# Kernel optimization log

Measured on AMD Instinct MI355X. Metric: run time of the kernel, lower is better.

The kernel has to match this reference:

```python
import jax, jax.numpy as jnp
import numpy as np

N_PARENTS = 4096   # parent clusters
K = 32             # points decoded per cluster
NEIGH = 128        # neigh_dec_size
FEAT = 256         # input_size (per-parent feature dim passed through)


def setup_inputs() -> dict:
    key = jax.random.key(0)
    ks = jax.random.split(key, 6)
    def lin(k, fan_in, fan_out):
        return jax.random.normal(k, (fan_in, fan_out), jnp.float32) / np.sqrt(fan_in).astype(np.float32)
    return {
        "input_features": jax.random.normal(ks[0], (N_PARENTS, NEIGH + FEAT), jnp.float32),
        # neighborhood decoder: Linear NEIGH -> K*3 (relative points)
        "W_dec": lin(ks[1], NEIGH, K * 3), "b_dec": jnp.zeros((K * 3,), jnp.float32),
        # fc chain: (FEAT+3) -> 512 -> 512 -> 256
        "W1": lin(ks[2], FEAT + 3, 512), "b1": jnp.zeros((512,), jnp.float32),
        "W2": lin(ks[3], 512, 512),      "b2": jnp.zeros((512,), jnp.float32),
        "W3": lin(ks[4], 512, 256),      "b3": jnp.zeros((256,), jnp.float32),
    }


def reference(input_features, W_dec, b_dec, W1, b1, W2, b2, W3, b3):
    # split: first NEIGH dims go to the neighborhood decoder, rest are parent features
    neigh_feats = input_features[:, :NEIGH]            # [N, NEIGH]
    features = input_features[:, NEIGH:]               # [N, FEAT]

    # neighborhood_dec: decode K relative 3D points per parent + cluster assignment
    relative_points = (neigh_feats @ W_dec + b_dec).reshape(-1, 3)   # [N*K, 3]
    cluster = jnp.repeat(jnp.arange(N_PARENTS, dtype=jnp.int32), K)  # [N*K]

    # gather parent features per point, concat with relative points
    features_dup = features[cluster]                                  # [N*K, FEAT]
    h = jnp.concatenate([features_dup, relative_points], axis=1)      # [N*K, FEAT+3]

    # chained Linear + ReLU (leaky=False)
    h = jax.nn.relu(h @ W1 + b1)
    h = jax.nn.relu(h @ W2 + b2)
    h = jax.nn.relu(h @ W3 + b3)
    return relative_points, h, cluster
```

## Files before the change

kernel.cpp:

```cpp
#include <hip/hip_runtime.h>
#include <hip/hip_bf16.h>

typedef unsigned short u16;
typedef unsigned int   u32;

#define NP     4096
#define NCH    131072
#define HBASE  393216
#define CLBASE 33947648

#define WS_W2F   0
#define WS_W3F   524288
#define WS_F1    1048576

using bf16x8 = __attribute__((ext_vector_type(8))) short;
using f32x4  = __attribute__((ext_vector_type(4))) float;

__device__ inline u32 pk2(float a, float b) {
  __hip_bfloat162 h = __float22bfloat162_rn(make_float2(a, b));
  return *reinterpret_cast<u32*>(&h);
}

__device__ inline int swz(int r, int cg) {
  return cg ^ (r & 7) ^ ((r >> 3) & 3);
}

__global__ __launch_bounds__(512, 2) void k_pre(const float* __restrict__ in_feats,
                                                const float* __restrict__ Wd,
                                                const float* __restrict__ bd,
                                                const float* __restrict__ W1,
                                                const float* __restrict__ b1,
                                                const float* __restrict__ W2,
                                                const float* __restrict__ W3,
                                                u16* __restrict__ w2f,
                                                u16* __restrict__ w3f,
                                                float* __restrict__ F1,
                                                float* __restrict__ out) {
  __shared__ __align__(16) char smem[69504];
  int b = blockIdx.x, tid = threadIdx.x;

  if (b < 256) {
    u16*   sh_a = (u16*)smem;
    float* b1s  = (float*)(smem + 8192);
    float* wdT  = (float*)(smem + 10240);
    float* ne   = (float*)(smem + 60928);
    float* bds  = (float*)(smem + 69120);
    int p0 = b * 16, lane = tid & 63, w = tid >> 6;
    b1s[tid] = b1[tid];
    if (tid < 96) bds[tid] = bd[tid];
    {
      int r = tid >> 5, k4 = (tid & 31) * 4;
      *(float4*)(ne + r * 128 + k4) = *(const float4*)(in_feats + (p0 + r) * 384 + k4);
    }
    {
      int r = tid >> 5, k0 = (tid & 31) * 8;
      const float4 v0 = *(const float4*)(in_feats + (p0 + r) * 384 + 128 + k0);
      const float4 v1 = *(const float4*)(in_feats + (p0 + r) * 384 + 128 + k0 + 4);
      uint4 o;
      o.x = pk2(v0.x, v0.y); o.y = pk2(v0.z, v0.w);
      o.z = pk2(v1.x, v1.y); o.w = pk2(v1.z, v1.w);
      int slot = (k0 >> 3) ^ (r & 7);
      *(uint4*)(sh_a + r * 256 + slot * 8) = o;
    }
    {
#pragma unroll
      for (int i = 0; i < 6; ++i) {
        int idx = i * 512 + tid;
        int k = idx / 24, c4 = (idx % 24) * 4;
        const float4 v = *(const float4*)(Wd + k * 96 + c4);
        wdT[(c4 + 0) * 132 + k] = v.x;
        wdT[(c4 + 1) * 132 + k] = v.y;
        wdT[(c4 + 2) * 132 + k] = v.z;
        wdT[(c4 + 3) * 132 + k] = v.w;
      }
    }
    __syncthreads();
#pragma unroll
    for (int j = 0; j < 3; ++j) {
      int u = j * 512 + tid;
      int p = u / 96, c = u - p * 96;
      const float4* nep = (const float4*)(ne + p * 128);
      const float4* wp  = (const float4*)(wdT + c * 132);
      float4 a4 = {0.f, 0.f, 0.f, 0.f};
#pragma unroll 8
      for (int kq = 0; kq < 32; ++kq) {
        const float4 av = nep[kq], bv = wp[kq];
        a4.x += av.x * bv.x; a4.y += av.y * bv.y;
        a4.z += av.z * bv.z; a4.w += av.w * bv.w;
      }
      out[(p0 + p) * 96 + c] = bds[c] + ((a4.x + a4.y) + (a4.z + a4.w));
    }
    f32x4 acc[4];
#pragma unroll
    for (int i = 0; i < 4; ++i) acc[i] = f32x4{0.f, 0.f, 0.f, 0.f};
    int col = lane & 15, q8 = (lane >> 4) * 8;
#pragma unroll
    for (int kc = 0; kc < 8; ++kc) {
      int slot = ((kc * 32 + q8) >> 3) ^ (col & 7);
      bf16x8 a = *(const bf16x8*)(sh_a + col * 256 + slot * 8);
#pragma unroll
      for (int nf = 0; nf < 4; ++nf) {
        const float* wp = W1 + (kc * 32 + q8) * 512 + (w * 4 + nf) * 16 + col;
        float v0 = wp[0],      v1 = wp[512],  v2 = wp[1024], v3 = wp[1536];
        float v4 = wp[2048],   v5 = wp[2560], v6 = wp[3072], v7 = wp[3584];
        union { bf16x8 v; u32 u[4]; } uu;
        uu.u[0] = pk2(v0, v1); uu.u[1] = pk2(v2, v3);
        uu.u[2] = pk2(v4, v5); uu.u[3] = pk2(v6, v7);
        acc[nf] = __builtin_amdgcn_mfma_f32_16x16x32_bf16(a, uu.v, acc[nf], 0, 0, 0);
      }
    }
    int rb = (lane >> 4) * 4;
#pragma unroll
    for (int nf = 0; nf < 4; ++nf) {
      int n = w * 64 + nf * 16 + col;
#pragma unroll
      for (int i = 0; i < 4; ++i)
        F1[(p0 + rb + i) * 512 + n] = acc[nf][i] + b1s[n];
    }
  } else if (b < 448) {
    float (*tile)[32][33] = (float (*)[32][33])smem;
    int h = tid >> 8, t = tid & 255;
    const float* src; u16* dst; int pitchN, g;
    if (b < 384) { g = (b - 256) * 2 + h; src = W2; dst = w2f; pitchN = 512; }
    else         { g = (b - 384) * 2 + h; src = W3; dst = w3f; pitchN = 256; }
    int kt = g & 15, nt = g >> 4;
    {
      int kk = t >> 3, n4 = (t & 7) * 4;
      const float4 v = *(const float4*)(src + (kt * 32 + kk) * pitchN + nt * 32 + n4);
      tile[h][kk][n4 + 0] = v.x; tile[h][kk][n4 + 1] = v.y;
      tile[h][kk][n4 + 2] = v.z; tile[h][kk][n4 + 3] = v.w;
    }
    __syncthreads();
    {
      int s = t >> 1, half = t & 1, fr = s >> 6, l = s & 63;
      int n_l = fr * 16 + (l & 15);
      int k_l = (l >> 4) * 8 + half * 4;
      uint2 o;
      o.x = pk2(tile[h][k_l + 0][n_l], tile[h][k_l + 1][n_l]);
      o.y = pk2(tile[h][k_l + 2][n_l], tile[h][k_l + 3][n_l]);
      int frag_id = (nt * 2 + fr) * 16 + kt;
      *(uint2*)(dst + frag_id * 512 + l * 8 + half * 4) = o;
    }
  } else {
    int idx = ((b - 448) * 512 + tid) * 4;
    float c = (float)(idx >> 5);
    float* p = out + CLBASE + idx;
    __builtin_nontemporal_store(c, p + 0);
    __builtin_nontemporal_store(c, p + 1);
    __builtin_nontemporal_store(c, p + 2);
    __builtin_nontemporal_store(c, p + 3);
  }
}

__global__ __launch_bounds__(512, 4) void k_main(const float* __restrict__ W1,
                                                 const float* __restrict__ b2,
                                                 const float* __restrict__ b3,
                                                 const u16* __restrict__ w2f,
                                                 const u16* __restrict__ w3f,
                                                 const float* __restrict__ F1,
                                                 float* __restrict__ out) {
  int blk = blockIdx.x;
  int tid = threadIdx.x, lane = tid & 63, w = tid >> 6;
  __shared__ u16 sh_h[64 * 512];
  __shared__ float f1s[1024], w1bs[1536], b2s[512], b3s[256], rels[192];

  f1s[tid]       = F1[blk * 1024 + tid];
  f1s[tid + 512] = F1[blk * 1024 + 512 + tid];
  w1bs[tid]        = W1[131072 + tid];
  w1bs[tid + 512]  = W1[131072 + 512 + tid];
  w1bs[tid + 1024] = W1[131072 + 1024 + tid];
  b2s[tid] = b2[tid];
  if (tid < 256) b3s[tid] = b3[tid];
  if (tid < 192) rels[tid] = out[blk * 192 + tid];
  __syncthreads();

  {
    int r = tid & 31, g = tid >> 5;
#pragma unroll
    for (int rr = 0; rr < 64; rr += 32) {
      int row = rr + r, pp = rr >> 5;
      float r0 = rels[row * 3 + 0], r1 = rels[row * 3 + 1], r2 = rels[row * 3 + 2];
#pragma unroll
      for (int gg = 0; gg < 4; ++gg) {
        int c8 = g * 8 + gg * 128;
        const float4 fa = *(const float4*)(f1s + pp * 512 + c8);
        const float4 fb = *(const float4*)(f1s + pp * 512 + c8 + 4);
        const float4 wa0 = *(const float4*)(w1bs + c8);
        const float4 wb0 = *(const float4*)(w1bs + c8 + 4);
        const float4 wa1 = *(const float4*)(w1bs + 512 + c8);
        const float4 wb1 = *(const float4*)(w1bs + 512 + c8 + 4);
        const float4 wa2 = *(const float4*)(w1bs + 1024 + c8);
        const float4 wb2 = *(const float4*)(w1bs + 1024 + c8 + 4);
        float v0 = fmaxf(fa.x + r0 * wa0.x + r1 * wa1.x + r2 * wa2.x, 0.f);
        float v1 = fmaxf(fa.y + r0 * wa0.y + r1 * wa1.y + r2 * wa2.y, 0.f);
        float v2 = fmaxf(fa.z + r0 * wa0.z + r1 * wa1.z + r2 * wa2.z, 0.f);
        float v3 = fmaxf(fa.w + r0 * wa0.w + r1 * wa1.w + r2 * wa2.w, 0.f);
        float v4 = fmaxf(fb.x + r0 * wb0.x + r1 * wb1.x + r2 * wb2.x, 0.f);
        float v5 = fmaxf(fb.y + r0 * wb0.y + r1 * wb1.y + r2 * wb2.y, 0.f);
        float v6 = fmaxf(fb.z + r0 * wb0.z + r1 * wb1.z + r2 * wb2.z, 0.f);
        float v7 = fmaxf(fb.w + r0 * wb0.w + r1 * wb1.w + r2 * wb2.w, 0.f);
        uint4 o;
        o.x = pk2(v0, v1); o.y = pk2(v2, v3);
        o.z = pk2(v4, v5); o.w = pk2(v6, v7);
        *(uint4*)(sh_h + row * 512 + swz(row, c8 >> 3) * 8) = o;
      }
    }
  }
  __syncthreads();

  int col = lane & 15, q8 = (lane >> 4) * 8;

  f32x4 acc2[4][4];
#pragma unroll
  for (int mf = 0; mf < 4; ++mf)
#pragma unroll
    for (int nf = 0; nf < 4; ++nf) acc2[mf][nf] = f32x4{0.f, 0.f, 0.f, 0.f};
  {
    const u16* w2p = w2f + (size_t)(w * 4 * 16) * 512 + lane * 8;
    bf16x8 bufA[4], bufB[4];
#pragma unroll
    for (int nf = 0; nf < 4; ++nf) bufA[nf] = *(const bf16x8*)(w2p + nf * 16 * 512);
#pragma unroll 2
    for (int kc = 0; kc < 16; ++kc) {
      const bf16x8* cur = (kc & 1) ? bufB : bufA;
      bf16x8* nxt = (kc & 1) ? bufA : bufB;
      if (kc < 15) {
#pragma unroll
        for (int nf = 0; nf < 4; ++nf)
          nxt[nf] = *(const bf16x8*)(w2p + (nf * 16 + kc + 1) * 512);
      }
      int cb = (kc * 32 + q8) >> 3;
#pragma unroll
      for (int mf = 0; mf < 4; ++mf) {
        int row = mf * 16 + col;
        bf16x8 a = *(const bf16x8*)(sh_h + row * 512 + swz(row, cb) * 8);
#pragma unroll
        for (int nf = 0; nf < 4; ++nf)
          acc2[mf][nf] = __builtin_amdgcn_mfma_f32_16x16x32_bf16(a, cur[nf], acc2[mf][nf], 0, 0, 0);
      }
    }
  }
  __syncthreads();

  {
    int rq = (lane >> 4) * 4;
#pragma unroll
    for (int mf = 0; mf < 4; ++mf)
#pragma unroll
      for (int nf = 0; nf < 4; ++nf) {
        int n = w * 64 + nf * 16 + col, cg = n >> 3, n7 = n & 7;
        float bv = b2s[n];
#pragma unroll
        for (int i = 0; i < 4; i += 2) {
          int r0 = mf * 16 + rq + i, r1 = r0 + 1;
          u32 p = pk2(fmaxf(acc2[mf][nf][i] + bv, 0.f),
                      fmaxf(acc2[mf][nf][i + 1] + bv, 0.f));
          sh_h[r0 * 512 + swz(r0, cg) * 8 + n7] = (u16)(p & 0xffff);
          sh_h[r1 * 512 + swz(r1, cg) * 8 + n7] = (u16)(p >> 16);
        }
      }
  }
  __syncthreads();

  f32x4 acc3[4][2];
#pragma unroll
  for (int mf = 0; mf < 4; ++mf)
#pragma unroll
    for (int nf = 0; nf < 2; ++nf) acc3[mf][nf] = f32x4{0.f, 0.f, 0.f, 0.f};
  {
    const u16* w3p = w3f + (size_t)(w * 2 * 16) * 512 + lane * 8;
    bf16x8 bufA[2], bufB[2];
#pragma unroll
    for (int nf = 0; nf < 2; ++nf) bufA[nf] = *(const bf16x8*)(w3p + nf * 16 * 512);
#pragma unroll 2
    for (int kc = 0; kc < 16; ++kc) {
      const bf16x8* cur = (kc & 1) ? bufB : bufA;
      bf16x8* nxt = (kc & 1) ? bufA : bufB;
      if (kc < 15) {
#pragma unroll
        for (int nf = 0; nf < 2; ++nf)
          nxt[nf] = *(const bf16x8*)(w3p + (nf * 16 + kc + 1) * 512);
      }
      int cb = (kc * 32 + q8) >> 3;
#pragma unroll
      for (int mf = 0; mf < 4; ++mf) {
        int row = mf * 16 + col;
        bf16x8 a = *(const bf16x8*)(sh_h + row * 512 + swz(row, cb) * 8);
#pragma unroll
        for (int nf = 0; nf < 2; ++nf)
          acc3[mf][nf] = __builtin_amdgcn_mfma_f32_16x16x32_bf16(a, cur[nf], acc3[mf][nf], 0, 0, 0);
      }
    }
  }

  {
    int rq = (lane >> 4) * 4;
#pragma unroll
    for (int mf = 0; mf < 4; ++mf)
#pragma unroll
      for (int nf = 0; nf < 2; ++nf) {
        int n = w * 32 + nf * 16 + col;
        float bv = b3s[n];
#pragma unroll
        for (int i = 0; i < 4; ++i) {
          int r = mf * 16 + rq + i;
          float v = fmaxf(acc3[mf][nf][i] + bv, 0.f);
          __builtin_nontemporal_store(v, out + HBASE + (blk * 64 + r) * 256 + n);
        }
      }
  }
}

extern "C" void kernel_launch(void* const* d_in, const int* in_sizes, int n_in,
                              void* d_out, int out_size, void* d_ws, size_t ws_size,
                              hipStream_t stream) {
  const float* in_feats = (const float*)d_in[0];
  const float* Wd = (const float*)d_in[1];
  const float* bd = (const float*)d_in[2];
  const float* W1 = (const float*)d_in[3];
  const float* b1 = (const float*)d_in[4];
  const float* W2 = (const float*)d_in[5];
  const float* b2 = (const float*)d_in[6];
  const float* W3 = (const float*)d_in[7];
  const float* b3 = (const float*)d_in[8];
  float* out = (float*)d_out;
  char* ws = (char*)d_ws;
  u16*   w2f = (u16*)(ws + WS_W2F);
  u16*   w3f = (u16*)(ws + WS_W3F);
  float* F1  = (float*)(ws + WS_F1);

  k_pre<<<512, 512, 0, stream>>>(in_feats, Wd, bd, W1, b1, W2, W3, w2f, w3f, F1, out);
  k_main<<<2048, 512, 0, stream>>>(W1, b2, b3, w2f, w3f, F1, out);
}
```

Before: 317.5 us.

## Double rows per block and build layer-1 activations per k-chunk inside layer-2 loop

Each block now handles 128 rows instead of 64, so every W2/W3 fragment fetched from global memory feeds twice as many MFMAs. The layer-1 activations are no longer built for the whole tile up front. Each 32-wide k-slice is built into small double-buffered LDS staging buffers inside the layer-2 loop, which overlaps that ALU work with the MFMAs. The cost is larger LDS use (about 158KB per block), twice the accumulator registers, a barrier on every k-step, bf16 rounding of the F1 features, and half as many blocks.

After: 288.2 us. 9.2% less time.

```diff
diff --git a/kernel.cpp b/kernel.cpp
--- a/kernel.cpp
+++ b/kernel.cpp
@@ -20,6 +20,8 @@
   __hip_bfloat162 h = __float22bfloat162_rn(make_float2(a, b));
   return *reinterpret_cast<u32*>(&h);
 }
+__device__ inline float bflo(u32 u) { union { u32 x; float f; } v; v.x = u << 16;        return v.f; }
+__device__ inline float bfhi(u32 u) { union { u32 x; float f; } v; v.x = u & 0xffff0000u; return v.f; }
 
 __device__ inline int swz(int r, int cg) {
   return cg ^ (r & 7) ^ ((r >> 3) & 3);
@@ -152,67 +154,73 @@
   }
 }
 
-__global__ __launch_bounds__(512, 4) void k_main(const float* __restrict__ W1,
+__global__ __launch_bounds__(512, 2) void k_main(const float* __restrict__ W1,
                                                  const float* __restrict__ b2,
                                                  const float* __restrict__ b3,
                                                  const u16* __restrict__ w2f,
                                                  const u16* __restrict__ w3f,
                                                  const float* __restrict__ F1,
                                                  float* __restrict__ out) {
+  __shared__ __align__(16) char smem[162304];
+  u16*   sh_h2 = (u16*)smem;
+  u16*   sb0   = (u16*)(smem + 131072);
+  u16*   sb1   = (u16*)(smem + 139264);
+  u16*   f1b   = (u16*)(smem + 147456);
+  float* w1bs  = (float*)(smem + 151552);
+  float* b2s   = (float*)(smem + 157696);
+  float* b3s   = (float*)(smem + 159744);
+  float* rels  = (float*)(smem + 160768);
+
   int blk = blockIdx.x;
   int tid = threadIdx.x, lane = tid & 63, w = tid >> 6;
-  __shared__ u16 sh_h[64 * 512];
-  __shared__ float f1s[1024], w1bs[1536], b2s[512], b3s[256], rels[192];
-
-  f1s[tid]       = F1[blk * 1024 + tid];
-  f1s[tid + 512] = F1[blk * 1024 + 512 + tid];
+  int col = lane & 15, q = lane >> 4, q8 = q * 8;
+
+  {
+    const float4 v = *(const float4*)(F1 + blk * 2048 + tid * 4);
+    uint2 o; o.x = pk2(v.x, v.y); o.y = pk2(v.z, v.w);
+    *(uint2*)(f1b + tid * 4) = o;
+  }
   w1bs[tid]        = W1[131072 + tid];
   w1bs[tid + 512]  = W1[131072 + 512 + tid];
   w1bs[tid + 1024] = W1[131072 + 1024 + tid];
   b2s[tid] = b2[tid];
   if (tid < 256) b3s[tid] = b3[tid];
-  if (tid < 192) rels[tid] = out[blk * 192 + tid];
+  if (tid < 384) rels[tid] = out[blk * 384 + tid];
   __syncthreads();
 
-  {
-    int r = tid & 31, g = tid >> 5;
-#pragma unroll
-    for (int rr = 0; rr < 64; rr += 32) {
-      int row = rr + r, pp = rr >> 5;
-      float r0 = rels[row * 3 + 0], r1 = rels[row * 3 + 1], r2 = rels[row * 3 + 2];
-#pragma unroll
-      for (int gg = 0; gg < 4; ++gg) {
-        int c8 = g * 8 + gg * 128;
-        const float4 fa = *(const float4*)(f1s + pp * 512 + c8);
-        const float4 fb = *(const float4*)(f1s + pp * 512 + c8 + 4);
-        const float4 wa0 = *(const float4*)(w1bs + c8);
-        const float4 wb0 = *(const float4*)(w1bs + c8 + 4);
-        const float4 wa1 = *(const float4*)(w1bs + 512 + c8);
-        const float4 wb1 = *(const float4*)(w1bs + 512 + c8 + 4);
-        const float4 wa2 = *(const float4*)(w1bs + 1024 + c8);
-        const float4 wb2 = *(const float4*)(w1bs + 1024 + c8 + 4);
-        float v0 = fmaxf(fa.x + r0 * wa0.x + r1 * wa1.x + r2 * wa2.x, 0.f);
-        float v1 = fmaxf(fa.y + r0 * wa0.y + r1 * wa1.y + r2 * wa2.y, 0.f);
-        float v2 = fmaxf(fa.z + r0 * wa0.z + r1 * wa1.z + r2 * wa2.z, 0.f);
-        float v3 = fmaxf(fa.w + r0 * wa0.w + r1 * wa1.w + r2 * wa2.w, 0.f);
-        float v4 = fmaxf(fb.x + r0 * wb0.x + r1 * wb1.x + r2 * wb2.x, 0.f);
-        float v5 = fmaxf(fb.y + r0 * wb0.y + r1 * wb1.y + r2 * wb2.y, 0.f);
-        float v6 = fmaxf(fb.z + r0 * wb0.z + r1 * wb1.z + r2 * wb2.z, 0.f);
-        float v7 = fmaxf(fb.w + r0 * wb0.w + r1 * wb1.w + r2 * wb2.w, 0.f);
-        uint4 o;
-        o.x = pk2(v0, v1); o.y = pk2(v2, v3);
-        o.z = pk2(v4, v5); o.w = pk2(v6, v7);
-        *(uint4*)(sh_h + row * 512 + swz(row, c8 >> 3) * 8) = o;
-      }
-    }
-  }
+  auto BUILD = [&](int ks, u16* sb) {
+    int row = tid >> 2, g = tid & 3;
+    int colG = ks * 32 + g * 8;
+    int p = row >> 5;
+    float r0 = rels[row * 3 + 0], r1 = rels[row * 3 + 1], r2 = rels[row * 3 + 2];
+    const uint4 fu = *(const uint4*)(f1b + p * 512 + colG);
+    const float4 wa0 = *(const float4*)(w1bs + colG);
+    const float4 wb0 = *(const float4*)(w1bs + colG + 4);
+    const float4 wa1 = *(const float4*)(w1bs + 512 + colG);
+    const float4 wb1 = *(const float4*)(w1bs + 512 + colG + 4);
+    const float4 wa2 = *(const float4*)(w1bs + 1024 + colG);
+    const float4 wb2 = *(const float4*)(w1bs + 1024 + colG + 4);
+    float v0 = fmaxf(bflo(fu.x) + r0 * wa0.x + r1 * wa1.x + r2 * wa2.x, 0.f);
+    float v1 = fmaxf(bfhi(fu.x) + r0 * wa0.y + r1 * wa1.y + r2 * wa2.y, 0.f);
+    float v2 = fmaxf(bflo(fu.y) + r0 * wa0.z + r1 * wa1.z + r2 * wa2.z, 0.f);
+    float v3 = fmaxf(bfhi(fu.y) + r0 * wa0.w + r1 * wa1.w + r2 * wa2.w, 0.f);
+    float v4 = fmaxf(bflo(fu.z) + r0 * wb0.x + r1 * wb1.x + r2 * wb2.x, 0.f);
+    float v5 = fmaxf(bfhi(fu.z) + r0 * wb0.y + r1 * wb1.y + r2 * wb2.y, 0.f);
+    float v6 = fmaxf(bflo(fu.w) + r0 * wb0.z + r1 * wb1.z + r2 * wb2.z, 0.f);
+    float v7 = fmaxf(bfhi(fu.w) + r0 * wb0.w + r1 * wb1.w + r2 * wb2.w, 0.f);
+    uint4 o;
+    o.x = pk2(v0, v1); o.y = pk2(v2, v3);
+    o.z = pk2(v4, v5); o.w = pk2(v6, v7);
+    int pg = g ^ ((row >> 1) & 3);
+    *(uint4*)(sb + row * 32 + pg * 8) = o;
+  };
+
+  BUILD(0, sb0);
   __syncthreads();
 
-  int col = lane & 15, q8 = (lane >> 4) * 8;
-
-  f32x4 acc2[4][4];
-#pragma unroll
-  for (int mf = 0; mf < 4; ++mf)
+  f32x4 acc2[8][4];
+#pragma unroll
+  for (int mf = 0; mf < 8; ++mf)
 #pragma unroll
     for (int nf = 0; nf < 4; ++nf) acc2[mf][nf] = f32x4{0.f, 0.f, 0.f, 0.f};
   {
@@ -220,32 +228,33 @@
     bf16x8 bufA[4], bufB[4];
 #pragma unroll
     for (int nf = 0; nf < 4; ++nf) bufA[nf] = *(const bf16x8*)(w2p + nf * 16 * 512);
-#pragma unroll 2
     for (int kc = 0; kc < 16; ++kc) {
       const bf16x8* cur = (kc & 1) ? bufB : bufA;
       bf16x8* nxt = (kc & 1) ? bufA : bufB;
+      u16* sbc = (kc & 1) ? sb1 : sb0;
+      u16* sbn = (kc & 1) ? sb0 : sb1;
       if (kc < 15) {
 #pragma unroll
         for (int nf = 0; nf < 4; ++nf)
           nxt[nf] = *(const bf16x8*)(w2p + (nf * 16 + kc + 1) * 512);
-      }
-      int cb = (kc * 32 + q8) >> 3;
-#pragma unroll
-      for (int mf = 0; mf < 4; ++mf) {
-        int row = mf * 16 + col;
-        bf16x8 a = *(const bf16x8*)(sh_h + row * 512 + swz(row, cb) * 8);
+        BUILD(kc + 1, sbn);
+      }
+#pragma unroll
+      for (int mf = 0; mf < 8; ++mf) {
+        int r = mf * 16 + col;
+        bf16x8 a = *(const bf16x8*)(sbc + r * 32 + ((q ^ ((r >> 1) & 3)) << 3));
 #pragma unroll
         for (int nf = 0; nf < 4; ++nf)
           acc2[mf][nf] = __builtin_amdgcn_mfma_f32_16x16x32_bf16(a, cur[nf], acc2[mf][nf], 0, 0, 0);
       }
-    }
-  }
-  __syncthreads();
-
-  {
-    int rq = (lane >> 4) * 4;
-#pragma unroll
-    for (int mf = 0; mf < 4; ++mf)
+      __syncthreads();
+    }
+  }
+
+  {
+    int rq = q * 4;
+#pragma unroll
+    for (int mf = 0; mf < 8; ++mf)
 #pragma unroll
       for (int nf = 0; nf < 4; ++nf) {
         int n = w * 64 + nf * 16 + col, cg = n >> 3, n7 = n & 7;
@@ -255,16 +264,16 @@
           int r0 = mf * 16 + rq + i, r1 = r0 + 1;
           u32 p = pk2(fmaxf(acc2[mf][nf][i] + bv, 0.f),
                       fmaxf(acc2[mf][nf][i + 1] + bv, 0.f));
-          sh_h[r0 * 512 + swz(r0, cg) * 8 + n7] = (u16)(p & 0xffff);
-          sh_h[r1 * 512 + swz(r1, cg) * 8 + n7] = (u16)(p >> 16);
+          sh_h2[r0 * 512 + swz(r0, cg) * 8 + n7] = (u16)(p & 0xffff);
+          sh_h2[r1 * 512 + swz(r1, cg) * 8 + n7] = (u16)(p >> 16);
         }
       }
   }
   __syncthreads();
 
-  f32x4 acc3[4][2];
-#pragma unroll
-  for (int mf = 0; mf < 4; ++mf)
+  f32x4 acc3[8][2];
+#pragma unroll
+  for (int mf = 0; mf < 8; ++mf)
 #pragma unroll
     for (int nf = 0; nf < 2; ++nf) acc3[mf][nf] = f32x4{0.f, 0.f, 0.f, 0.f};
   {
@@ -283,9 +292,9 @@
       }
       int cb = (kc * 32 + q8) >> 3;
 #pragma unroll
-      for (int mf = 0; mf < 4; ++mf) {
-        int row = mf * 16 + col;
-        bf16x8 a = *(const bf16x8*)(sh_h + row * 512 + swz(row, cb) * 8);
+      for (int mf = 0; mf < 8; ++mf) {
+        int r = mf * 16 + col;
+        bf16x8 a = *(const bf16x8*)(sh_h2 + r * 512 + swz(r, cb) * 8);
 #pragma unroll
         for (int nf = 0; nf < 2; ++nf)
           acc3[mf][nf] = __builtin_amdgcn_mfma_f32_16x16x32_bf16(a, cur[nf], acc3[mf][nf], 0, 0, 0);
@@ -294,9 +303,9 @@
   }
 
   {
-    int rq = (lane >> 4) * 4;
-#pragma unroll
-    for (int mf = 0; mf < 4; ++mf)
+    int rq = q * 4;
+#pragma unroll
+    for (int mf = 0; mf < 8; ++mf)
 #pragma unroll
       for (int nf = 0; nf < 2; ++nf) {
         int n = w * 32 + nf * 16 + col;
@@ -305,7 +314,7 @@
         for (int i = 0; i < 4; ++i) {
           int r = mf * 16 + rq + i;
           float v = fmaxf(acc3[mf][nf][i] + bv, 0.f);
-          __builtin_nontemporal_store(v, out + HBASE + (blk * 64 + r) * 256 + n);
+          __builtin_nontemporal_store(v, out + HBASE + (blk * 128 + r) * 256 + n);
         }
       }
   }
@@ -330,5 +339,5 @@
   float* F1  = (float*)(ws + WS_F1);
 
   k_pre<<<512, 512, 0, stream>>>(in_feats, Wd, bd, W1, b1, W2, W3, w2f, w3f, F1, out);
-  k_main<<<2048, 512, 0, stream>>>(W1, b2, b3, w2f, w3f, F1, out);
-}
+  k_main<<<1024, 512, 0, stream>>>(W1, b2, b3, w2f, w3f, F1, out);
+}
```

## Double block row tile to 128 rows with 16 waves sharing weight fragments

Applied to the files above, without the earlier changes.

Each block now handles 128 points (4 parents) using 1024 threads arranged as 2 row-groups by 8 column-groups of waves. Each W2/W3 column slice is fetched by two waves instead of once per 64-row block, halving the number of blocks that stream the weight fragments from global/L2. The trade-off is double the LDS per block (about 150KB), which limits occupancy to one block per CU and may hurt latency hiding.

Result: faster. 267.1 us (-15.9%).

```diff
diff --git a/kernel.cpp b/kernel.cpp
--- a/kernel.cpp
+++ b/kernel.cpp
@@ -152,71 +152,68 @@
   }
 }
 
-__global__ __launch_bounds__(512, 4) void k_main(const float* __restrict__ W1,
-                                                 const float* __restrict__ b2,
-                                                 const float* __restrict__ b3,
-                                                 const u16* __restrict__ w2f,
-                                                 const u16* __restrict__ w3f,
-                                                 const float* __restrict__ F1,
-                                                 float* __restrict__ out) {
+__global__ __launch_bounds__(1024) void k_main(const float* __restrict__ W1,
+                                               const float* __restrict__ b2,
+                                               const float* __restrict__ b3,
+                                               const u16* __restrict__ w2f,
+                                               const u16* __restrict__ w3f,
+                                               const float* __restrict__ F1,
+                                               float* __restrict__ out) {
   int blk = blockIdx.x;
   int tid = threadIdx.x, lane = tid & 63, w = tid >> 6;
-  __shared__ u16 sh_h[64 * 512];
-  __shared__ float f1s[1024], w1bs[1536], b2s[512], b3s[256], rels[192];
-
-  f1s[tid]       = F1[blk * 1024 + tid];
-  f1s[tid + 512] = F1[blk * 1024 + 512 + tid];
-  w1bs[tid]        = W1[131072 + tid];
-  w1bs[tid + 512]  = W1[131072 + 512 + tid];
-  w1bs[tid + 1024] = W1[131072 + 1024 + tid];
-  b2s[tid] = b2[tid];
-  if (tid < 256) b3s[tid] = b3[tid];
-  if (tid < 192) rels[tid] = out[blk * 192 + tid];
+  int wm = w >> 3, wn = w & 7;
+  int col = lane & 15, q = lane >> 4, q8 = q * 8;
+  __shared__ u16 sh_h[128 * 512];
+  __shared__ float f1s[2048], w1bs[1536], b2s[512], b3s[256], rels[384];
+
+  if (tid < 512) *(float4*)(f1s + tid * 4) = *(const float4*)(F1 + blk * 2048 + tid * 4);
+  if (tid < 768) *(float2*)(w1bs + tid * 2) = *(const float2*)(W1 + 131072 + tid * 2);
+  if (tid < 512) b2s[tid] = b2[tid];
+  if (tid >= 512 && tid < 768) b3s[tid - 512] = b3[tid - 512];
+  if (tid >= 768 && tid < 1024) {
+    float2 rv = *(const float2*)(out + blk * 384 + (tid - 768) * 2);
+    rels[(tid - 768) * 2 + 0] = rv.x;
+    rels[(tid - 768) * 2 + 1] = rv.y;
+  }
   __syncthreads();
 
   {
-    int r = tid & 31, g = tid >> 5;
-#pragma unroll
-    for (int rr = 0; rr < 64; rr += 32) {
-      int row = rr + r, pp = rr >> 5;
-      float r0 = rels[row * 3 + 0], r1 = rels[row * 3 + 1], r2 = rels[row * 3 + 2];
-#pragma unroll
-      for (int gg = 0; gg < 4; ++gg) {
-        int c8 = g * 8 + gg * 128;
-        const float4 fa = *(const float4*)(f1s + pp * 512 + c8);
-        const float4 fb = *(const float4*)(f1s + pp * 512 + c8 + 4);
-        const float4 wa0 = *(const float4*)(w1bs + c8);
-        const float4 wb0 = *(const float4*)(w1bs + c8 + 4);
-        const float4 wa1 = *(const float4*)(w1bs + 512 + c8);
-        const float4 wb1 = *(const float4*)(w1bs + 512 + c8 + 4);
-        const float4 wa2 = *(const float4*)(w1bs + 1024 + c8);
-        const float4 wb2 = *(const float4*)(w1bs + 1024 + c8 + 4);
-        float v0 = fmaxf(fa.x + r0 * wa0.x + r1 * wa1.x + r2 * wa2.x, 0.f);
-        float v1 = fmaxf(fa.y + r0 * wa0.y + r1 * wa1.y + r2 * wa2.y, 0.f);
-        float v2 = fmaxf(fa.z + r0 * wa0.z + r1 * wa1.z + r2 * wa2.z, 0.f);
-        float v3 = fmaxf(fa.w + r0 * wa0.w + r1 * wa1.w + r2 * wa2.w, 0.f);
-        float v4 = fmaxf(fb.x + r0 * wb0.x + r1 * wb1.x + r2 * wb2.x, 0.f);
-        float v5 = fmaxf(fb.y + r0 * wb0.y + r1 * wb1.y + r2 * wb2.y, 0.f);
-        float v6 = fmaxf(fb.z + r0 * wb0.z + r1 * wb1.z + r2 * wb2.z, 0.f);
-        float v7 = fmaxf(fb.w + r0 * wb0.w + r1 * wb1.w + r2 * wb2.w, 0.f);
-        uint4 o;
-        o.x = pk2(v0, v1); o.y = pk2(v2, v3);
-        o.z = pk2(v4, v5); o.w = pk2(v6, v7);
-        *(uint4*)(sh_h + row * 512 + swz(row, c8 >> 3) * 8) = o;
-      }
+    int row = tid >> 3, g = tid & 7, pp = row >> 5;
+    float r0 = rels[row * 3 + 0], r1 = rels[row * 3 + 1], r2 = rels[row * 3 + 2];
+#pragma unroll
+    for (int j = 0; j < 8; ++j) {
+      int c8 = g * 8 + j * 64;
+      const float4 fa = *(const float4*)(f1s + pp * 512 + c8);
+      const float4 fb = *(const float4*)(f1s + pp * 512 + c8 + 4);
+      const float4 wa0 = *(const float4*)(w1bs + c8);
+      const float4 wb0 = *(const float4*)(w1bs + c8 + 4);
+      const float4 wa1 = *(const float4*)(w1bs + 512 + c8);
+      const float4 wb1 = *(const float4*)(w1bs + 512 + c8 + 4);
+      const float4 wa2 = *(const float4*)(w1bs + 1024 + c8);
+      const float4 wb2 = *(const float4*)(w1bs + 1024 + c8 + 4);
+      float v0 = fmaxf(fa.x + r0 * wa0.x + r1 * wa1.x + r2 * wa2.x, 0.f);
+      float v1 = fmaxf(fa.y + r0 * wa0.y + r1 * wa1.y + r2 * wa2.y, 0.f);
+      float v2 = fmaxf(fa.z + r0 * wa0.z + r1 * wa1.z + r2 * wa2.z, 0.f);
+      float v3 = fmaxf(fa.w + r0 * wa0.w + r1 * wa1.w + r2 * wa2.w, 0.f);
+      float v4 = fmaxf(fb.x + r0 * wb0.x + r1 * wb1.x + r2 * wb2.x, 0.f);
+      float v5 = fmaxf(fb.y + r0 * wb0.y + r1 * wb1.y + r2 * wb2.y, 0.f);
+      float v6 = fmaxf(fb.z + r0 * wb0.z + r1 * wb1.z + r2 * wb2.z, 0.f);
+      float v7 = fmaxf(fb.w + r0 * wb0.w + r1 * wb1.w + r2 * wb2.w, 0.f);
+      uint4 o;
+      o.x = pk2(v0, v1); o.y = pk2(v2, v3);
+      o.z = pk2(v4, v5); o.w = pk2(v6, v7);
+      *(uint4*)(sh_h + row * 512 + swz(row, c8 >> 3) * 8) = o;
     }
   }
   __syncthreads();
 
-  int col = lane & 15, q8 = (lane >> 4) * 8;
-
   f32x4 acc2[4][4];
 #pragma unroll
   for (int mf = 0; mf < 4; ++mf)
 #pragma unroll
     for (int nf = 0; nf < 4; ++nf) acc2[mf][nf] = f32x4{0.f, 0.f, 0.f, 0.f};
   {
-    const u16* w2p = w2f + (size_t)(w * 4 * 16) * 512 + lane * 8;
+    const u16* w2p = w2f + (size_t)(wn * 4 * 16) * 512 + lane * 8;
     bf16x8 bufA[4], bufB[4];
 #pragma unroll
     for (int nf = 0; nf < 4; ++nf) bufA[nf] = *(const bf16x8*)(w2p + nf * 16 * 512);
@@ -232,8 +229,8 @@
       int cb = (kc * 32 + q8) >> 3;
 #pragma unroll
       for (int mf = 0; mf < 4; ++mf) {
-        int row = mf * 16 + col;
-        bf16x8 a = *(const bf16x8*)(sh_h + row * 512 + swz(row, cb) * 8);
+        int r = wm * 64 + mf * 16 + col;
+        bf16x8 a = *(const bf16x8*)(sh_h + r * 512 + swz(r, cb) * 8);
 #pragma unroll
         for (int nf = 0; nf < 4; ++nf)
           acc2[mf][nf] = __builtin_amdgcn_mfma_f32_16x16x32_bf16(a, cur[nf], acc2[mf][nf], 0, 0, 0);
@@ -243,16 +240,16 @@
   __syncthreads();
 
   {
-    int rq = (lane >> 4) * 4;
+    int rq = q * 4;
 #pragma unroll
     for (int mf = 0; mf < 4; ++mf)
 #pragma unroll
       for (int nf = 0; nf < 4; ++nf) {
-        int n = w * 64 + nf * 16 + col, cg = n >> 3, n7 = n & 7;
+        int n = wn * 64 + nf * 16 + col, cg = n >> 3, n7 = n & 7;
         float bv = b2s[n];
 #pragma unroll
         for (int i = 0; i < 4; i += 2) {
-          int r0 = mf * 16 + rq + i, r1 = r0 + 1;
+          int r0 = wm * 64 + mf * 16 + rq + i, r1 = r0 + 1;
           u32 p = pk2(fmaxf(acc2[mf][nf][i] + bv, 0.f),
                       fmaxf(acc2[mf][nf][i + 1] + bv, 0.f));
           sh_h[r0 * 512 + swz(r0, cg) * 8 + n7] = (u16)(p & 0xffff);
@@ -268,7 +265,7 @@
 #pragma unroll
     for (int nf = 0; nf < 2; ++nf) acc3[mf][nf] = f32x4{0.f, 0.f, 0.f, 0.f};
   {
-    const u16* w3p = w3f + (size_t)(w * 2 * 16) * 512 + lane * 8;
+    const u16* w3p = w3f + (size_t)(wn * 2 * 16) * 512 + lane * 8;
     bf16x8 bufA[2], bufB[2];
 #pragma unroll
     for (int nf = 0; nf < 2; ++nf) bufA[nf] = *(const bf16x8*)(w3p + nf * 16 * 512);
@@ -284,8 +281,8 @@
       int cb = (kc * 32 + q8) >> 3;
 #pragma unroll
       for (int mf = 0; mf < 4; ++mf) {
-        int row = mf * 16 + col;
-        bf16x8 a = *(const bf16x8*)(sh_h + row * 512 + swz(row, cb) * 8);
+        int r = wm * 64 + mf * 16 + col;
+        bf16x8 a = *(const bf16x8*)(sh_h + r * 512 + swz(r, cb) * 8);
 #pragma unroll
         for (int nf = 0; nf < 2; ++nf)
           acc3[mf][nf] = __builtin_amdgcn_mfma_f32_16x16x32_bf16(a, cur[nf], acc3[mf][nf], 0, 0, 0);
@@ -294,18 +291,18 @@
   }
 
   {
-    int rq = (lane >> 4) * 4;
+    int rq = q * 4;
 #pragma unroll
     for (int mf = 0; mf < 4; ++mf)
 #pragma unroll
       for (int nf = 0; nf < 2; ++nf) {
-        int n = w * 32 + nf * 16 + col;
+        int n = wn * 32 + nf * 16 + col;
         float bv = b3s[n];
 #pragma unroll
         for (int i = 0; i < 4; ++i) {
-          int r = mf * 16 + rq + i;
+          int r = wm * 64 + mf * 16 + rq + i;
           float v = fmaxf(acc3[mf][nf][i] + bv, 0.f);
-          __builtin_nontemporal_store(v, out + HBASE + (blk * 64 + r) * 256 + n);
+          __builtin_nontemporal_store(v, out + HBASE + (blk * 128 + r) * 256 + n);
         }
       }
   }
@@ -330,5 +327,5 @@
   float* F1  = (float*)(ws + WS_F1);
 
   k_pre<<<512, 512, 0, stream>>>(in_feats, Wd, bd, W1, b1, W2, W3, w2f, w3f, F1, out);
-  k_main<<<2048, 512, 0, stream>>>(W1, b2, b3, w2f, w3f, F1, out);
-}
+  k_main<<<1024, 1024, 0, stream>>>(W1, b2, b3, w2f, w3f, F1, out);
+}
```
